# Kernel tuning notes

Measured on AMD Instinct MI355X. Metric: run time of the kernel, lower is better.

Reference implementation:

```python
import jax, jax.numpy as jnp
import numpy as np

NUM_HEADS = 8
BLOCK = 8      # block_size
HALO = 2       # kernel_size (halo width)


def _rel_to_abs(rel):
    # halo-style relative->absolute conversion
    # rel: [B, G, qh, qw, 2*p-1] -> [B, G, qh, qw, p]
    B, G, qh, qw, dim = rel.shape
    p = (dim + 1) // 2
    gap = p - qw
    flat = rel.reshape(B, G, qh, qw * dim)[:, :, :, qw - 1:-1]
    return flat.reshape(B, G, qh, qw, 2 * (p - 1))[:, :, :, :, gap:p + gap]


def _relative_logits(pos_q, pos_emb_h, pos_emb_w):
    # pos_q: [B, G, qb, qb, kd]; pos_emb_*: [kd, 2*p-1]
    rel_w = _rel_to_abs(jnp.einsum('bghwd,dr->bghwr', pos_q, pos_emb_w))  # [B,G,qb,qb,p] key-width
    q_t = pos_q.transpose(0, 1, 3, 2, 4)
    rel_h = _rel_to_abs(jnp.einsum('bgwhd,dr->bgwhr', q_t, pos_emb_h))
    rel_h = rel_h.transpose(0, 1, 3, 2, 4)  # [B,G,qb,qb,p] key-height
    return rel_h[..., :, None] + rel_w[..., None, :]  # [B,G,qb,qb,p,p]


def reference(x, w_q, w_kv, w_out, pos_emb_h, pos_emb_w):
    B, H, W, C = x.shape
    kd = C // NUM_HEADS                # per-head key dim
    kvk = BLOCK + 2 * HALO             # halo window size
    out_ch = w_out.shape[1]
    v_dim = out_ch // NUM_HEADS
    kv_per_head = (C + out_ch) // NUM_HEADS
    hh, ww = H // BLOCK, W // BLOCK
    scale = float(1.0 / np.sqrt(kd))

    # ---- query (1x1 conv == matmul), blockify ----
    q = (x @ w_q).reshape(B, hh, BLOCK, ww, BLOCK, NUM_HEADS, kd)
    q = q.transpose(0, 5, 1, 3, 2, 4, 6)  # [B,nh,hh,ww,qb,qb,kd]
    attn_q = q.reshape(B, NUM_HEADS, hh, ww, BLOCK * BLOCK, kd) * scale
    pos_q = q.reshape(B, NUM_HEADS * hh * ww, BLOCK, BLOCK, kd)

    # ---- key/value: 1x1 conv, halo pad, unfold into overlapping windows ----
    kv = jnp.pad(x @ w_kv, ((0, 0), (HALO, HALO), (HALO, HALO), (0, 0)))
    idx = np.arange(hh)[:, None] * BLOCK + np.arange(kvk)[None, :]  # [hh,kvk]
    idy = np.arange(ww)[:, None] * BLOCK + np.arange(kvk)[None, :]  # [ww,kvk]
    patches = kv[:, idx][:, :, :, idy]           # [B,hh,kvk,ww,kvk,kv_dim]
    patches = patches.transpose(0, 1, 3, 2, 4, 5)  # [B,hh,ww,kvk,kvk,kv_dim]
    kvh = patches.reshape(B, hh, ww, kvk, kvk, NUM_HEADS, kv_per_head)
    kvh = kvh.transpose(0, 5, 1, 2, 3, 4, 6).reshape(B, NUM_HEADS, hh, ww, kvk * kvk, kv_per_head)
    key, value = kvh[..., :kd], kvh[..., kd:]

    # ---- attention with relative position bias ----
    scores = jnp.einsum('bnhwqd,bnhwkd->bnhwqk', attn_q, key)
    pos = _relative_logits(pos_q, pos_emb_h, pos_emb_w)
    pos = pos.reshape(B, NUM_HEADS, hh, ww, BLOCK * BLOCK, kvk * kvk)
    attn = jax.nn.softmax(scores + pos, axis=-1)
    out = jnp.einsum('bnhwqk,bnhwkv->bnhwqv', attn, value)  # [B,nh,hh,ww,qb*qb,v_dim]

    # ---- de-blockify, output projection ----
    out = out.reshape(B, NUM_HEADS, hh, ww, BLOCK, BLOCK, v_dim)
    out = out.transpose(0, 2, 4, 3, 5, 1, 6).reshape(B, H, W, NUM_HEADS * v_dim)
    return out @ w_out


def setup_inputs() -> dict:
    key = jax.random.key(0)
    ks = jax.random.split(key, 6)
    B, H, W, C = 4, 128, 128, 256
    out_ch = 256
    kd = C // NUM_HEADS
    kvk = BLOCK + 2 * HALO
    std = kd ** -0.5
    return {
        'x': jax.random.normal(ks[0], (B, H, W, C), jnp.float32),
        'w_q': jax.random.normal(ks[1], (C, C), jnp.float32) * 0.02,
        'w_kv': jax.random.normal(ks[2], (C, C + out_ch), jnp.float32) * 0.02,
        'w_out': jax.random.normal(ks[3], (C, out_ch), jnp.float32) * 0.02,
        'pos_emb_h': jax.random.normal(ks[4], (kd, 2 * kvk - 1), jnp.float32) * std,
        'pos_emb_w': jax.random.normal(ks[5], (kd, 2 * kvk - 1), jnp.float32) * std,
    }
```

## Files before the change

kernel.cpp:

```cpp
#include <hip/hip_runtime.h>
#include <hip/hip_bf16.h>
#include <cstdint>


#define KVK 12
#define NKEYS 144
#define VT_S 160
#define PT_S 168
#define LOG2E 1.4426950408889634f

typedef unsigned int u32;
typedef unsigned long long u64;
typedef unsigned short u16;
typedef __attribute__((ext_vector_type(8))) __bf16 bf16x8;
typedef __attribute__((ext_vector_type(4))) float f32x4;

__device__ __forceinline__ u16 f2bf(float f) {
    u32 x = __float_as_uint(f);
    return (u16)((x + 0x7fffu + ((x >> 16) & 1u)) >> 16);
}
__device__ __forceinline__ u32 cvtpk(float lo, float hi) {
    u32 d;
    asm("v_cvt_pk_bf16_f32 %0, %1, %2" : "=v"(d) : "v"(lo), "v"(hi));
    return d;
}
__device__ __forceinline__ float max3f(float a, float b, float c) {
    float d;
    asm("v_max3_f32 %0, %1, %2, %3" : "=v"(d) : "v"(a), "v"(b), "v"(c));
    return d;
}
__device__ __forceinline__ float exp2a(float x) {
    float d;
    asm("v_exp_f32 %0, %1" : "=v"(d) : "v"(x));
    return d;
}
__device__ __forceinline__ void gload16(const void* g, void* l) {
    __builtin_amdgcn_global_load_lds(
        (const __attribute__((address_space(1))) void*)g,
        (__attribute__((address_space(3))) void*)l, 16, 0, 0);
}
__device__ __forceinline__ u32 pack2(float lo, float hi) {
    return (u32)f2bf(lo) | ((u32)f2bf(hi) << 16);
}

__global__ __launch_bounds__(256) void conv_prep(const float* __restrict__ x,
                                                 u16* __restrict__ xb,
                                                 const float* __restrict__ wq,
                                                 const float* __restrict__ wkv,
                                                 const float* __restrict__ wout,
                                                 u16* __restrict__ wT,
                                                 u16* __restrict__ woutT,
                                                 const float* __restrict__ emb_h,
                                                 const float* __restrict__ emb_w,
                                                 u16* __restrict__ embT) {
    int blk = blockIdx.x, t = threadIdx.x;
    if (blk < 8192) {
        int i = blk * 256 + t;
        const float4* p = reinterpret_cast<const float4*>(x) + (long)i * 2;
        float4 a = p[0], b = p[1];
        uint4 o;
        o.x = pack2(a.x, a.y); o.y = pack2(a.z, a.w);
        o.z = pack2(b.x, b.y); o.w = pack2(b.z, b.w);
        reinterpret_cast<uint4*>(xb)[i] = o;
        return;
    }
    blk -= 8192;
    if (blk < 256) {
        int idx = blk * 256 + t; int nn = idx >> 8, k = idx & 255;
        wT[idx] = f2bf(wq[(long)k * 256 + nn]);
    } else if (blk < 768) {
        int idx = (blk - 256) * 256 + t; int nn = idx >> 8, k = idx & 255;
        float v = wkv[(long)k * 512 + nn];
        if ((nn & 32) == 0) v *= 0.2550348642f;
        wT[65536 + idx] = f2bf(v);
    } else if (blk < 1024) {
        int idx = (blk - 768) * 256 + t; int nn = idx >> 8, k = idx & 255;
        woutT[idx] = f2bf(wout[(long)k * 256 + nn]);
    } else if (blk == 1024) {
        for (int i = t; i < 1024; i += 256) {
            int p = i >> 5, d = i & 31;
            embT[i] = (p < 23) ? f2bf(emb_h[d * 23 + p]) : 0;
        }
    } else {
        for (int i = t; i < 1024; i += 256) {
            int p = i >> 5, d = i & 31;
            embT[1024 + i] = (p < 23) ? f2bf(emb_w[d * 23 + p]) : 0;
        }
    }
}

__global__ __launch_bounds__(256) void gemm_qkv6(const u16* __restrict__ A,
                                                 const u16* __restrict__ WT,
                                                 u16* __restrict__ Qb,
                                                 u16* __restrict__ KVb) {
    __shared__ u16 As[8192];
    __shared__ u16 Bs[8192];
    const int t = threadIdx.x;
    const int bid = blockIdx.x;
    const int mIdx = (bid / 48) * 8 + (bid & 7);
    const int nt = (bid >> 3) % 6;
    const int w = t >> 6, lane = t & 63;
    const long m0 = (long)mIdx * 128;
    const long n0 = (long)nt * 128;
    const int wr = w >> 1, wc = w & 1;
    const int r = lane & 15, g = lane >> 4;

    f32x4 acc[4][4];
    #pragma unroll
    for (int i = 0; i < 4; ++i)
        #pragma unroll
        for (int j = 0; j < 4; ++j) acc[i][j] = (f32x4){0.f, 0.f, 0.f, 0.f};

    const u16* Ags[4];
    const u16* Bgs[4];
    #pragma unroll
    for (int cq = 0; cq < 4; ++cq) {
        int u = cq * 256 + w * 64 + lane;
        int panel = u >> 9, row = (u >> 2) & 127, col8 = (u & 3) * 8;
        Ags[cq] = A + (m0 + row) * 256 + panel * 32 + col8;
        Bgs[cq] = WT + (n0 + row) * 256 + panel * 32 + col8;
    }

    for (int k0 = 0; k0 < 256; k0 += 64) {
        #pragma unroll
        for (int cq = 0; cq < 4; ++cq) {
            gload16(Ags[cq] + k0, &As[cq * 2048 + w * 512]);
            gload16(Bgs[cq] + k0, &Bs[cq * 2048 + w * 512]);
        }
        __syncthreads();
        #pragma unroll
        for (int kk = 0; kk < 2; ++kk) {
            bf16x8 a[4], b[4];
            #pragma unroll
            for (int i = 0; i < 4; ++i)
                a[i] = *reinterpret_cast<const bf16x8*>(
                    &As[kk * 4096 + (wr * 64 + i * 16 + r) * 32 + g * 8]);
            #pragma unroll
            for (int j = 0; j < 4; ++j)
                b[j] = *reinterpret_cast<const bf16x8*>(
                    &Bs[kk * 4096 + (wc * 64 + j * 16 + r) * 32 + g * 8]);
            #pragma unroll
            for (int i = 0; i < 4; ++i)
                #pragma unroll
                for (int j = 0; j < 4; ++j)
                    acc[i][j] = __builtin_amdgcn_mfma_f32_16x16x32_bf16(b[j], a[i], acc[i][j], 0, 0, 0);
        }
        __syncthreads();
    }

    const bool isQ = (nt < 2);
    #pragma unroll
    for (int i = 0; i < 4; ++i) {
        long row = m0 + wr * 64 + i * 16 + r;
        #pragma unroll
        for (int j = 0; j < 4; ++j) {
            long colb = n0 + wc * 64 + j * 16 + g * 4;
            uint2 st;
            st.x = cvtpk(acc[i][j][0], acc[i][j][1]);
            st.y = cvtpk(acc[i][j][2], acc[i][j][3]);
            if (isQ) *reinterpret_cast<uint2*>(Qb + row * 256 + colb) = st;
            else     *reinterpret_cast<uint2*>(KVb + row * 512 + colb - 256) = st;
        }
    }
}

__global__ __launch_bounds__(256) void mfma_gemm(const u16* __restrict__ A,
                                                 const u16* __restrict__ BT,
                                                 float* __restrict__ C, int N) {
    __shared__ u16 As[8192];
    __shared__ u16 Bs[8192];
    const int t = threadIdx.x;
    const int bid = blockIdx.x;
    const int mIdx = (bid / 16) * 8 + (bid & 7);
    const int nt = (bid >> 3) & 1;
    const int w = t >> 6, lane = t & 63;
    const long m0 = (long)mIdx * 128;
    const long n0 = (long)nt * 128;
    const int wr = w >> 1, wc = w & 1;
    const int r = lane & 15, g = lane >> 4;

    f32x4 acc[4][4];
    #pragma unroll
    for (int i = 0; i < 4; ++i)
        #pragma unroll
        for (int j = 0; j < 4; ++j) acc[i][j] = (f32x4){0.f, 0.f, 0.f, 0.f};

    const u16* Ags[4];
    const u16* Bgs[4];
    #pragma unroll
    for (int cq = 0; cq < 4; ++cq) {
        int u = cq * 256 + w * 64 + lane;
        int panel = u >> 9, row = (u >> 2) & 127, col8 = (u & 3) * 8;
        Ags[cq] = A + (m0 + row) * 256 + panel * 32 + col8;
        Bgs[cq] = BT + (n0 + row) * 256 + panel * 32 + col8;
    }

    for (int k0 = 0; k0 < 256; k0 += 64) {
        #pragma unroll
        for (int cq = 0; cq < 4; ++cq) {
            gload16(Ags[cq] + k0, &As[cq * 2048 + w * 512]);
            gload16(Bgs[cq] + k0, &Bs[cq * 2048 + w * 512]);
        }
        __syncthreads();
        #pragma unroll
        for (int kk = 0; kk < 2; ++kk) {
            bf16x8 a[4], b[4];
            #pragma unroll
            for (int i = 0; i < 4; ++i)
                a[i] = *reinterpret_cast<const bf16x8*>(
                    &As[kk * 4096 + (wr * 64 + i * 16 + r) * 32 + g * 8]);
            #pragma unroll
            for (int j = 0; j < 4; ++j)
                b[j] = *reinterpret_cast<const bf16x8*>(
                    &Bs[kk * 4096 + (wc * 64 + j * 16 + r) * 32 + g * 8]);
            #pragma unroll
            for (int i = 0; i < 4; ++i)
                #pragma unroll
                for (int j = 0; j < 4; ++j)
                    acc[i][j] = __builtin_amdgcn_mfma_f32_16x16x32_bf16(b[j], a[i], acc[i][j], 0, 0, 0);
        }
        __syncthreads();
    }

    #pragma unroll
    for (int i = 0; i < 4; ++i) {
        long row = m0 + wr * 64 + i * 16 + r;
        #pragma unroll
        for (int j = 0; j < 4; ++j) {
            long colb = n0 + wc * 64 + j * 16 + g * 4;
            float4 st = make_float4(acc[i][j][0], acc[i][j][1], acc[i][j][2], acc[i][j][3]);
            *reinterpret_cast<float4*>(C + row * N + colb) = st;
        }
    }
}

#define UNITLOAD(U, VK, VV, KD, VB) {                                          \
    int kk_ = (U) >> 2, p_ = (U) & 3;                                          \
    int ky_ = (kk_ * 171) >> 11, kx_ = kk_ - 12 * ky_;                         \
    int gy_ = by * 8 + ky_ - 2, gx_ = bx * 8 + kx_ - 2;                        \
    if (((unsigned)gy_ < 128u) && ((unsigned)gx_ < 128u)) {                    \
        const u16* bp_ = KVb + (((long)b * 128 + gy_) * 128 + gx_) * 512 + n * 64 + p_ * 8; \
        VK = *reinterpret_cast<const uint4*>(bp_);                             \
        VV = *reinterpret_cast<const uint4*>(bp_ + 32);                        \
    }                                                                          \
    KD = kk_ * 64 + ((p_ * 8) ^ ((kk_ & 7) << 3));                             \
    VB = (p_ * 8) * VT_S + (kk_ ^ (p_ << 3));                                  \
}
#define VSCAT(VV, VB) {                                                        \
    u16 tmp_[8];                                                               \
    *reinterpret_cast<uint4*>(tmp_) = VV;                                      \
    _Pragma("unroll")                                                          \
    for (int i_ = 0; i_ < 8; ++i_) Vt[(VB) + i_ * VT_S] = tmp_[i_];            \
}

__global__ __launch_bounds__(256, 5) void attn_mfma(const u16* __restrict__ Qb,
                                                    const u16* __restrict__ KVb,
                                                    const u16* __restrict__ embT,
                                                    u16* __restrict__ Ob) {
    __shared__ __align__(16) char blob[22528];
    u16* Ks  = (u16*)blob;
    u16* Qe  = (u16*)(blob + 18432);
    u16* PT  = (u16*)blob;
    __shared__ u16 Vt[32 * VT_S];

    const int gblk = blockIdx.x;
    const int n = gblk & 7;
    const int bx = (gblk >> 3) & 15;
    const int by = (gblk >> 7) & 15;
    const int b = gblk >> 11;
    const int t = threadIdx.x;
    const int w = t >> 6, lane = t & 63;
    const int g = lane >> 4, r = lane & 15;

    const int q = w * 16 + r;
    const int qi = q >> 3, qj = q & 7;
    const long qrow = ((long)b * 128 + by * 8 + qi) * 128 + bx * 8 + qj;

    bf16x8 qa1 = *reinterpret_cast<const bf16x8*>(Qb + qrow * 256 + n * 32 + g * 8);
    bf16x8 ah0 = *reinterpret_cast<const bf16x8*>(embT + r * 32 + g * 8);
    bf16x8 ah1 = *reinterpret_cast<const bf16x8*>(embT + (16 + r) * 32 + g * 8);
    bf16x8 aw0 = *reinterpret_cast<const bf16x8*>(embT + 1024 + r * 32 + g * 8);
    bf16x8 aw1 = *reinterpret_cast<const bf16x8*>(embT + 1024 + (16 + r) * 32 + g * 8);

    uint4 z4 = make_uint4(0u, 0u, 0u, 0u);
    uint4 vK0 = z4, vV0 = z4, vK1 = z4, vV1 = z4, vK2 = z4, vV2 = z4;
    int kd0 = 0, vb0 = 0, kd1 = 0, vb1 = 0, kd2 = 0, vb2 = 0;
    UNITLOAD(t, vK0, vV0, kd0, vb0);
    UNITLOAD(t + 256, vK1, vV1, kd1, vb1);
    if (t < 64) UNITLOAD(t + 512, vK2, vV2, kd2, vb2);

    *reinterpret_cast<uint4*>(&Ks[kd0]) = vK0;
    *reinterpret_cast<uint4*>(&Ks[kd1]) = vK1;
    if (t < 64) *reinterpret_cast<uint4*>(&Ks[kd2]) = vK2;

    for (int u = t; u < 576; u += 256) {
        int kk = u >> 2, uu = u & 3;
        int ky = (kk * 171) >> 11;
        int kx = kk - 12 * ky;
        int hy = ky - 8 * uu;
        int hx = 12 + kx - 8 * uu;
        u64 lo = 0, hi = 0;
        if ((unsigned)hy < 4u) lo |= 0x3F80ULL << (hy * 16);
        else if ((unsigned)hy < 8u) hi |= 0x3F80ULL << ((hy - 4) * 16);
        if ((unsigned)hx < 4u) lo |= 0x3F80ULL << (hx * 16);
        else if ((unsigned)hx < 8u) hi |= 0x3F80ULL << ((hx - 4) * 16);
        int col = (32 + uu * 8) ^ ((kk & 7) << 3);
        u64* dst = reinterpret_cast<u64*>(&Ks[kk * 64 + col]);
        dst[0] = lo;
        dst[1] = hi;
    }
    if (t < 64) *reinterpret_cast<uint4*>(&Qe[t * 32 + 24]) = z4;
    if (t >= 224) {
        int d = t - 224;
        int sw = ((d >> 3) & 3) << 3;
        *reinterpret_cast<uint4*>(&Vt[d * VT_S + (144 ^ sw)]) = z4;
        *reinterpret_cast<uint4*>(&Vt[d * VT_S + (152 ^ sw)]) = z4;
    }

    {
        f32x4 z = (f32x4){0.f, 0.f, 0.f, 0.f};
        __builtin_amdgcn_s_setprio(1);
        f32x4 rh0 = __builtin_amdgcn_mfma_f32_16x16x32_bf16(ah0, qa1, z, 0, 0, 0);
        f32x4 rh1 = __builtin_amdgcn_mfma_f32_16x16x32_bf16(ah1, qa1, z, 0, 0, 0);
        f32x4 rw0 = __builtin_amdgcn_mfma_f32_16x16x32_bf16(aw0, qa1, z, 0, 0, 0);
        f32x4 rw1 = __builtin_amdgcn_mfma_f32_16x16x32_bf16(aw1, qa1, z, 0, 0, 0);
        __builtin_amdgcn_s_setprio(0);
        #pragma unroll
        for (int ti = 0; ti < 2; ++ti) {
            #pragma unroll
            for (int e = 0; e < 4; ++e) {
                int p = ti * 16 + g * 4 + e;
                float vh = (ti ? rh1[e] : rh0[e]) * LOG2E;
                float vw = (ti ? rw1[e] : rw0[e]) * LOG2E;
                int kyd = p + qi - 11;
                int kxd = p + qj - 11;
                if ((unsigned)kyd < 12u) Qe[q * 32 + kyd] = f2bf(vh);
                if ((unsigned)kxd < 12u) Qe[q * 32 + 12 + kxd] = f2bf(vw);
            }
        }
    }

    VSCAT(vV0, vb0);
    VSCAT(vV1, vb1);
    if (t < 64) VSCAT(vV2, vb2);

    __syncthreads();

    bf16x8 qa2 = *reinterpret_cast<const bf16x8*>(&Qe[q * 32 + g * 8]);
    f32x4 acc[9];
    __builtin_amdgcn_s_setprio(1);
    #pragma unroll
    for (int j = 0; j < 9; ++j) {
        int krow = j * 16 + r;
        int sw = (r & 7) << 3;
        bf16x8 kb0 = *reinterpret_cast<const bf16x8*>(&Ks[krow * 64 + ((g * 8) ^ sw)]);
        bf16x8 kb1 = *reinterpret_cast<const bf16x8*>(&Ks[krow * 64 + ((32 + g * 8) ^ sw)]);
        f32x4 z = (f32x4){0.f, 0.f, 0.f, 0.f};
        acc[j] = __builtin_amdgcn_mfma_f32_16x16x32_bf16(kb1, qa2,
                 __builtin_amdgcn_mfma_f32_16x16x32_bf16(kb0, qa1, z, 0, 0, 0), 0, 0, 0);
    }
    __builtin_amdgcn_s_setprio(0);

    float mx = max3f(acc[0][0], acc[0][1], acc[0][2]);
    mx = fmaxf(mx, acc[0][3]);
    #pragma unroll
    for (int j = 1; j < 9; ++j)
        mx = max3f(mx, max3f(acc[j][0], acc[j][1], acc[j][2]), acc[j][3]);
    mx = fmaxf(mx, __shfl_xor(mx, 16));
    mx = fmaxf(mx, __shfl_xor(mx, 32));
    float s0 = 0.f, s1 = 0.f, s2 = 0.f, s3 = 0.f;
    u32 pkA[9], pkB[9];
    #pragma unroll
    for (int j = 0; j < 9; ++j) {
        float e0 = exp2a(acc[j][0] - mx);
        float e1 = exp2a(acc[j][1] - mx);
        float e2 = exp2a(acc[j][2] - mx);
        float e3 = exp2a(acc[j][3] - mx);
        s0 += e0; s1 += e1; s2 += e2; s3 += e3;
        pkA[j] = cvtpk(e0, e1);
        pkB[j] = cvtpk(e2, e3);
    }
    float sum = (s0 + s1) + (s2 + s3);
    sum += __shfl_xor(sum, 16);
    sum += __shfl_xor(sum, 32);
    const float inv = __builtin_amdgcn_rcpf(sum);

    __syncthreads();

    {
        const int ptb = q * PT_S;
        #pragma unroll
        for (int j = 0; j < 9; ++j) {
            *reinterpret_cast<u32*>(&PT[ptb + 16 * j + 4 * g]) = pkA[j];
            *reinterpret_cast<u32*>(&PT[ptb + 16 * j + 4 * g + 2]) = pkB[j];
        }
    }
    if (t < 64) {
        *reinterpret_cast<uint4*>(&PT[t * PT_S + 144]) = make_uint4(0u, 0u, 0u, 0u);
        *reinterpret_cast<uint4*>(&PT[t * PT_S + 152]) = make_uint4(0u, 0u, 0u, 0u);
    }
    __syncthreads();

    const int sw0 = (r >> 3) << 3;
    const int sw1 = (2 + (r >> 3)) << 3;
    f32x4 o0 = (f32x4){0.f, 0.f, 0.f, 0.f};
    f32x4 o1 = (f32x4){0.f, 0.f, 0.f, 0.f};
    __builtin_amdgcn_s_setprio(1);
    #pragma unroll
    for (int kk = 0; kk < 5; ++kk) {
        bf16x8 pb = *reinterpret_cast<const bf16x8*>(&PT[q * PT_S + kk * 32 + g * 8]);
        bf16x8 va0 = *reinterpret_cast<const bf16x8*>(&Vt[r * VT_S + ((kk * 32 + g * 8) ^ sw0)]);
        bf16x8 va1 = *reinterpret_cast<const bf16x8*>(&Vt[(16 + r) * VT_S + ((kk * 32 + g * 8) ^ sw1)]);
        o0 = __builtin_amdgcn_mfma_f32_16x16x32_bf16(va0, pb, o0, 0, 0, 0);
        o1 = __builtin_amdgcn_mfma_f32_16x16x32_bf16(va1, pb, o1, 0, 0, 0);
    }
    __builtin_amdgcn_s_setprio(0);
    {
        uint2 st0, st1;
        st0.x = cvtpk(o0[0] * inv, o0[1] * inv);
        st0.y = cvtpk(o0[2] * inv, o0[3] * inv);
        st1.x = cvtpk(o1[0] * inv, o1[1] * inv);
        st1.y = cvtpk(o1[2] * inv, o1[3] * inv);
        *reinterpret_cast<uint2*>(Ob + qrow * 256 + n * 32 + g * 4) = st0;
        *reinterpret_cast<uint2*>(Ob + qrow * 256 + n * 32 + 16 + g * 4) = st1;
    }
}

extern "C" void kernel_launch(void* const* d_in, const int* in_sizes, int n_in,
                              void* d_out, int out_size, void* d_ws, size_t ws_size,
                              hipStream_t stream) {
    const float* x     = (const float*)d_in[0];
    const float* w_q   = (const float*)d_in[1];
    const float* w_kv  = (const float*)d_in[2];
    const float* w_out = (const float*)d_in[3];
    const float* emb_h = (const float*)d_in[4];
    const float* emb_w = (const float*)d_in[5];

    u16* xb = (u16*)d_out;
    u16* Qb = (u16*)((char*)d_out + (size_t)33554432);
    char* ws = (char*)d_ws;
    u16* KVb   = (u16*)(ws);
    u16* Ob    = (u16*)(ws + (size_t)67108864);
    u16* wT    = (u16*)(ws + (size_t)100663296);
    u16* woutT = (u16*)(ws + (size_t)100663296 + 393216);
    u16* embT  = (u16*)(ws + (size_t)100663296 + 524288);

    dim3 blk(256);
    conv_prep<<<dim3(9218), blk, 0, stream>>>(x, xb, w_q, w_kv, w_out, wT, woutT,
                                              emb_h, emb_w, embT);
    gemm_qkv6<<<dim3(3072), blk, 0, stream>>>(xb, wT, Qb, KVb);
    attn_mfma<<<dim3(8192), blk, 0, stream>>>(Qb, KVb, embT, Ob);
    mfma_gemm<<<dim3(1024), blk, 0, stream>>>(Ob, woutT, (float*)d_out, 256);
}
```

Baseline: 132.9 us.

## Fuse fp32-to-bf16 input conversion into QKV GEMM and precompute one-hot key table

```diff
diff --git a/kernel.cpp b/kernel.cpp
--- a/kernel.cpp
+++ b/kernel.cpp
@@ -14,6 +14,7 @@
 typedef unsigned short u16;
 typedef __attribute__((ext_vector_type(8))) __bf16 bf16x8;
 typedef __attribute__((ext_vector_type(4))) float f32x4;
+typedef __attribute__((ext_vector_type(4))) u32 u32x4;
 
 __device__ __forceinline__ u16 f2bf(float f) {
     u32 x = __float_as_uint(f);
@@ -39,32 +40,17 @@
         (const __attribute__((address_space(1))) void*)g,
         (__attribute__((address_space(3))) void*)l, 16, 0, 0);
 }
-__device__ __forceinline__ u32 pack2(float lo, float hi) {
-    return (u32)f2bf(lo) | ((u32)f2bf(hi) << 16);
-}
-
-__global__ __launch_bounds__(256) void conv_prep(const float* __restrict__ x,
-                                                 u16* __restrict__ xb,
-                                                 const float* __restrict__ wq,
+
+__global__ __launch_bounds__(256) void conv_prep(const float* __restrict__ wq,
                                                  const float* __restrict__ wkv,
                                                  const float* __restrict__ wout,
                                                  u16* __restrict__ wT,
                                                  u16* __restrict__ woutT,
                                                  const float* __restrict__ emb_h,
                                                  const float* __restrict__ emb_w,
-                                                 u16* __restrict__ embT) {
+                                                 u16* __restrict__ embT,
+                                                 u16* __restrict__ ohT) {
     int blk = blockIdx.x, t = threadIdx.x;
-    if (blk < 8192) {
-        int i = blk * 256 + t;
-        const float4* p = reinterpret_cast<const float4*>(x) + (long)i * 2;
-        float4 a = p[0], b = p[1];
-        uint4 o;
-        o.x = pack2(a.x, a.y); o.y = pack2(a.z, a.w);
-        o.z = pack2(b.x, b.y); o.w = pack2(b.z, b.w);
-        reinterpret_cast<uint4*>(xb)[i] = o;
-        return;
-    }
-    blk -= 8192;
     if (blk < 256) {
         int idx = blk * 256 + t; int nn = idx >> 8, k = idx & 255;
         wT[idx] = f2bf(wq[(long)k * 256 + nn]);
@@ -81,19 +67,35 @@
             int p = i >> 5, d = i & 31;
             embT[i] = (p < 23) ? f2bf(emb_h[d * 23 + p]) : 0;
         }
-    } else {
+    } else if (blk == 1025) {
         for (int i = t; i < 1024; i += 256) {
             int p = i >> 5, d = i & 31;
             embT[1024 + i] = (p < 23) ? f2bf(emb_w[d * 23 + p]) : 0;
         }
-    }
-}
-
-__global__ __launch_bounds__(256) void gemm_qkv6(const u16* __restrict__ A,
+    } else {
+        for (int u = t; u < 576; u += 256) {
+            int kk = u >> 2, uu = u & 3;
+            int ky = (kk * 171) >> 11;
+            int kx = kk - 12 * ky;
+            int hy = ky - 8 * uu;
+            int hx = 12 + kx - 8 * uu;
+            u64 lo = 0, hi = 0;
+            if ((unsigned)hy < 4u) lo |= 0x3F80ULL << (hy * 16);
+            else if ((unsigned)hy < 8u) hi |= 0x3F80ULL << ((hy - 4) * 16);
+            if ((unsigned)hx < 4u) lo |= 0x3F80ULL << (hx * 16);
+            else if ((unsigned)hx < 8u) hi |= 0x3F80ULL << ((hx - 4) * 16);
+            u64* dst = reinterpret_cast<u64*>(ohT) + (size_t)u * 2;
+            dst[0] = lo;
+            dst[1] = hi;
+        }
+    }
+}
+
+__global__ __launch_bounds__(256) void gemm_qkv6(const float* __restrict__ X,
                                                  const u16* __restrict__ WT,
                                                  u16* __restrict__ Qb,
                                                  u16* __restrict__ KVb) {
-    __shared__ u16 As[8192];
+    __shared__ float Asf[8192];
     __shared__ u16 Bs[8192];
     const int t = threadIdx.x;
     const int bid = blockIdx.x;
@@ -111,30 +113,46 @@
         #pragma unroll
         for (int j = 0; j < 4; ++j) acc[i][j] = (f32x4){0.f, 0.f, 0.f, 0.f};
 
-    const u16* Ags[4];
+    const float* Ags[8];
+    #pragma unroll
+    for (int cq = 0; cq < 8; ++cq) {
+        int D = cq * 256 + t;
+        int panel = D >> 10, row = (D >> 3) & 127, c4p = D & 7;
+        Ags[cq] = X + (m0 + row) * 256 + panel * 32 + ((c4p ^ (row & 7)) << 2);
+    }
     const u16* Bgs[4];
     #pragma unroll
     for (int cq = 0; cq < 4; ++cq) {
         int u = cq * 256 + w * 64 + lane;
         int panel = u >> 9, row = (u >> 2) & 127, col8 = (u & 3) * 8;
-        Ags[cq] = A + (m0 + row) * 256 + panel * 32 + col8;
         Bgs[cq] = WT + (n0 + row) * 256 + panel * 32 + col8;
     }
+    const int s7 = r & 7;
+    const int ph0 = (2 * g) ^ s7;
+    const int ph1 = (2 * g + 1) ^ s7;
+    const float4* Af4 = reinterpret_cast<const float4*>(Asf);
 
     for (int k0 = 0; k0 < 256; k0 += 64) {
         #pragma unroll
-        for (int cq = 0; cq < 4; ++cq) {
-            gload16(Ags[cq] + k0, &As[cq * 2048 + w * 512]);
+        for (int cq = 0; cq < 8; ++cq)
+            gload16(Ags[cq] + k0, &Asf[(cq * 256 + w * 64) * 4]);
+        #pragma unroll
+        for (int cq = 0; cq < 4; ++cq)
             gload16(Bgs[cq] + k0, &Bs[cq * 2048 + w * 512]);
-        }
         __syncthreads();
         #pragma unroll
         for (int kk = 0; kk < 2; ++kk) {
             bf16x8 a[4], b[4];
             #pragma unroll
-            for (int i = 0; i < 4; ++i)
-                a[i] = *reinterpret_cast<const bf16x8*>(
-                    &As[kk * 4096 + (wr * 64 + i * 16 + r) * 32 + g * 8]);
+            for (int i = 0; i < 4; ++i) {
+                int R = wr * 64 + i * 16 + r;
+                int sb = kk * 1024 + R * 8;
+                float4 f0 = Af4[sb + ph0];
+                float4 f1 = Af4[sb + ph1];
+                u32x4 pk = (u32x4){cvtpk(f0.x, f0.y), cvtpk(f0.z, f0.w),
+                                   cvtpk(f1.x, f1.y), cvtpk(f1.z, f1.w)};
+                a[i] = __builtin_bit_cast(bf16x8, pk);
+            }
             #pragma unroll
             for (int j = 0; j < 4; ++j)
                 b[j] = *reinterpret_cast<const bf16x8*>(
@@ -256,6 +274,7 @@
 __global__ __launch_bounds__(256, 5) void attn_mfma(const u16* __restrict__ Qb,
                                                     const u16* __restrict__ KVb,
                                                     const u16* __restrict__ embT,
+                                                    const u16* __restrict__ ohT,
                                                     u16* __restrict__ Ob) {
     __shared__ __align__(16) char blob[22528];
     u16* Ks  = (u16*)blob;
@@ -289,25 +308,26 @@
     UNITLOAD(t + 256, vK1, vV1, kd1, vb1);
     if (t < 64) UNITLOAD(t + 512, vK2, vV2, kd2, vb2);
 
+    const uint4* oh4 = reinterpret_cast<const uint4*>(ohT);
+    uint4 oh0 = oh4[t];
+    uint4 oh1 = oh4[t + 256];
+    uint4 oh2 = (t < 64) ? oh4[t + 512] : z4;
+
     *reinterpret_cast<uint4*>(&Ks[kd0]) = vK0;
     *reinterpret_cast<uint4*>(&Ks[kd1]) = vK1;
     if (t < 64) *reinterpret_cast<uint4*>(&Ks[kd2]) = vK2;
 
-    for (int u = t; u < 576; u += 256) {
-        int kk = u >> 2, uu = u & 3;
-        int ky = (kk * 171) >> 11;
-        int kx = kk - 12 * ky;
-        int hy = ky - 8 * uu;
-        int hx = 12 + kx - 8 * uu;
-        u64 lo = 0, hi = 0;
-        if ((unsigned)hy < 4u) lo |= 0x3F80ULL << (hy * 16);
-        else if ((unsigned)hy < 8u) hi |= 0x3F80ULL << ((hy - 4) * 16);
-        if ((unsigned)hx < 4u) lo |= 0x3F80ULL << (hx * 16);
-        else if ((unsigned)hx < 8u) hi |= 0x3F80ULL << ((hx - 4) * 16);
-        int col = (32 + uu * 8) ^ ((kk & 7) << 3);
-        u64* dst = reinterpret_cast<u64*>(&Ks[kk * 64 + col]);
-        dst[0] = lo;
-        dst[1] = hi;
+    {
+        int kk = t >> 2, uu = t & 3;
+        *reinterpret_cast<uint4*>(&Ks[kk * 64 + ((32 + uu * 8) ^ ((kk & 7) << 3))]) = oh0;
+        int u1 = t + 256;
+        kk = u1 >> 2; uu = u1 & 3;
+        *reinterpret_cast<uint4*>(&Ks[kk * 64 + ((32 + uu * 8) ^ ((kk & 7) << 3))]) = oh1;
+        if (t < 64) {
+            int u2 = t + 512;
+            kk = u2 >> 2; uu = u2 & 3;
+            *reinterpret_cast<uint4*>(&Ks[kk * 64 + ((32 + uu * 8) ^ ((kk & 7) << 3))]) = oh2;
+        }
     }
     if (t < 64) *reinterpret_cast<uint4*>(&Qe[t * 32 + 24]) = z4;
     if (t >= 224) {
@@ -436,19 +456,19 @@
     const float* emb_h = (const float*)d_in[4];
     const float* emb_w = (const float*)d_in[5];
 
-    u16* xb = (u16*)d_out;
-    u16* Qb = (u16*)((char*)d_out + (size_t)33554432);
+    u16* Qb = (u16*)d_out;
     char* ws = (char*)d_ws;
     u16* KVb   = (u16*)(ws);
     u16* Ob    = (u16*)(ws + (size_t)67108864);
     u16* wT    = (u16*)(ws + (size_t)100663296);
     u16* woutT = (u16*)(ws + (size_t)100663296 + 393216);
     u16* embT  = (u16*)(ws + (size_t)100663296 + 524288);
+    u16* ohT   = (u16*)(ws + (size_t)100663296 + 528384);
 
     dim3 blk(256);
-    conv_prep<<<dim3(9218), blk, 0, stream>>>(x, xb, w_q, w_kv, w_out, wT, woutT,
-                                              emb_h, emb_w, embT);
-    gemm_qkv6<<<dim3(3072), blk, 0, stream>>>(xb, wT, Qb, KVb);
-    attn_mfma<<<dim3(8192), blk, 0, stream>>>(Qb, KVb, embT, Ob);
+    conv_prep<<<dim3(1027), blk, 0, stream>>>(w_q, w_kv, w_out, wT, woutT,
+                                              emb_h, emb_w, embT, ohT);
+    gemm_qkv6<<<dim3(3072), blk, 0, stream>>>(x, wT, Qb, KVb);
+    attn_mfma<<<dim3(8192), blk, 0, stream>>>(Qb, KVb, embT, ohT, Ob);
     mfma_gemm<<<dim3(1024), blk, 0, stream>>>(Ob, woutT, (float*)d_out, 256);
 }
```

New measurement: 138.3 us. +4.1%, slower.
